# Optimization experiments

Measured on AMD Instinct MI355X. Metric: run time of the kernel, lower is better.

The kernel has to match this reference:

```python
import jax, jax.numpy as jnp
import numpy as np

# Constants matching module reset(): R_reset=5 -> R = 5+15 = 20; T = 10.0; kn=0, gn=1
G = 128          # grid_side
N = G * G        # 16384 cells
R = 20
NB = (2 * R + 3) ** 2        # 1849 = nb_neighbors per the module's assert
NSHIFT = (2 * R + 1) ** 2    # 1681 slots actually filled by the shift loop
T = 10.0
NB_RULES = 4


def _neighbor_idx():
    idx = np.arange(N)
    i, j = idx // G, idx % G
    si, sj = np.meshgrid(np.arange(-R, R + 1), np.arange(-R, R + 1), indexing='ij')
    si, sj = si.ravel(), sj.ravel()   # row-major: shift_i outer loop, shift_j inner
    nb = ((i[:, None] + si[None, :]) % G) * G + (j[:, None] + sj[None, :]) % G  # [N, NSHIFT]
    full = np.zeros((N, NB), dtype=np.int32)   # unfilled slots default to cell 0 (as in torch zeros init)
    full[:, :NSHIFT] = nb
    return jnp.asarray(full)

NEI = _neighbor_idx()   # [N, NB] int32, translation-invariant periodic neighbor list


def setup_inputs() -> dict:
    key = jax.random.key(0)
    ks = jax.random.split(key, 9)
    idx = jnp.arange(N)
    pos = jnp.stack([idx // G, idx % G], axis=-1).astype(jnp.float32)   # [N, 2] grid coords
    x = jax.random.uniform(ks[0], (N, 3), dtype=jnp.float32)            # [N, C] state in [0,1]
    c0 = jax.random.randint(ks[1], (NB_RULES,), 0, 3)                   # source channel per rule
    c1 = jax.random.randint(ks[2], (NB_RULES,), 0, 3)                   # target channel per rule
    r = 0.5 + 0.5 * jax.random.uniform(ks[3], (NB_RULES,), dtype=jnp.float32)
    rk = jax.random.uniform(ks[4], (NB_RULES, 3), dtype=jnp.float32)    # kernel ring centers
    b = jax.random.uniform(ks[5], (NB_RULES, 3), dtype=jnp.float32)     # kernel ring heights
    w = 0.1 + 0.4 * jax.random.uniform(ks[6], (NB_RULES, 3), dtype=jnp.float32)  # ring widths
    h = jax.random.uniform(ks[7], (NB_RULES,), dtype=jnp.float32)       # growth strength
    m = 0.1 + 0.4 * jax.random.uniform(ks[8], (NB_RULES,), dtype=jnp.float32)    # growth mean
    s = 0.05 + 0.1 * jax.random.uniform(jax.random.fold_in(key, 99), (NB_RULES,), dtype=jnp.float32)
    return {"pos": pos, "x": x, "c0": c0, "c1": c1, "r": r, "rk": rk,
            "b": b, "w": w, "h": h, "m": m, "s": s}


def reference(pos, x, c0, c1, r, rk, b, w, h, m, s):
    # gather neighbor states: x_ext[:, 0] is self, rest are the NB neighbors -> [N, 1+NB, C]
    x_ext = jnp.concatenate([x[:, None, :], x[NEI]], axis=1)
    # translation-invariant distance computed at the center cell (as in torch)
    center = G * G // 2 + G // 2
    dpos = jnp.concatenate([jnp.zeros((1, 2), pos.dtype), pos[NEI[center]] - pos[center]], axis=0)  # [1+NB, 2]
    dist = jnp.sqrt(jnp.sum(dpos ** 2, axis=-1)) / R   # [1+NB]
    edge_mask = jax.nn.sigmoid(-(dist - 1.0) * 10.0)
    delta_x = jnp.zeros_like(x)
    for k in range(NB_RULES):
        # kernel_core[0]: sum of Gaussian rings over the last axis
        wk = edge_mask * (b[k] * jnp.exp(-((dist[:, None] / r[k] - rk[k]) / w[k]) ** 2 / 2)).sum(-1)  # [1+NB]
        wn = wk / wk.sum()                    # per-cell weight rows are identical -> compute once
        potential = jnp.mean(wn[None, :] * x_ext[:, :, c0[k]], axis=1)   # aggr='mean' -> [N]
        # field_func[1]
        field = jnp.exp(-(potential - m[k]) ** 2 / (2 * s[k] ** 2) - 0.001) * 2 - 1
        delta_x = delta_x.at[:, c1[k]].add(h[k] * field)
    new_x = jnp.clip(x + delta_x / T, 0.0, 1.0)
    return pos, new_x
```

## Files before the change

### kernel.cpp

```cpp
#include <hip/hip_runtime.h>
#include <math.h>

#define G 128
#define NCELLS (G*G)
#define RAD 20
#define NS 41
#define NTAPS (NS*NS)
#define NB_FULL 1850.0f
#define NTAIL 168.0f
#define NRULES 4
#define NQ 16
#define SROWPAD 44
#define SSZ (NS*SROWPAD)
#define NTILES 16
#define CONV_BLOCKS (NTILES*NRULES*NQ)

#define WOFF_TAIL 0
#define WOFF_STEN 16
#define WOFF_POT  (WOFF_STEN + NRULES*SSZ)

__device__ __forceinline__ float kw(float d, float irk,
                                    float rk0, float rk1, float rk2,
                                    float b0, float b1, float b2,
                                    float iw0, float iw1, float iw2) {
    float em = 1.f / (1.f + __expf((d - 1.f) * 10.f));
    float dd = d * irk;
    float u0 = (dd - rk0) * iw0;
    float u1 = (dd - rk1) * iw1;
    float u2 = (dd - rk2) * iw2;
    return em * (b0 * __expf(-0.5f * u0 * u0)
               + b1 * __expf(-0.5f * u1 * u1)
               + b2 * __expf(-0.5f * u2 * u2));
}

__global__ __launch_bounds__(256)
void lenia_prep(const float* __restrict__ rr,
                const float* __restrict__ rkv,
                const float* __restrict__ bv,
                const float* __restrict__ wv,
                float* __restrict__ ws) {
    __shared__ float red[4];
    const int k = blockIdx.x;
    const int t = threadIdx.x;

    const float irk = 1.f / rr[k];
    const float rk0 = rkv[k*3+0], rk1 = rkv[k*3+1], rk2 = rkv[k*3+2];
    const float b0  = bv[k*3+0],  b1  = bv[k*3+1],  b2  = bv[k*3+2];
    const float iw0 = 1.f / wv[k*3+0], iw1 = 1.f / wv[k*3+1], iw2 = 1.f / wv[k*3+2];
    const float invR = 1.f / (float)RAD;

    float vals[7];
    float lsum = 0.f;
    #pragma unroll
    for (int j = 0; j < 7; ++j) {
        int sidx = t + j * 256;
        float wk = 0.f;
        if (sidx < NTAPS) {
            int si = sidx / NS - RAD;
            int sj = sidx % NS - RAD;
            float d = sqrtf((float)(si*si + sj*sj)) * invR;
            wk = kw(d, irk, rk0, rk1, rk2, b0, b1, b2, iw0, iw1, iw2);
        }
        vals[j] = wk;
        lsum += wk;
    }
    #pragma unroll
    for (int mm = 32; mm > 0; mm >>= 1) lsum += __shfl_xor(lsum, mm, 64);
    if ((t & 63) == 0) red[t >> 6] = lsum;
    __syncthreads();
    const float S4 = red[0] + red[1] + red[2] + red[3];
    const float wself = kw(0.f, irk, rk0, rk1, rk2, b0, b1, b2, iw0, iw1, iw2);
    const float dtail = sqrtf(8192.f) * invR;
    const float wtail = kw(dtail, irk, rk0, rk1, rk2, b0, b1, b2, iw0, iw1, iw2);
    const float S = S4 + wself + NTAIL * wtail;
    const float inv = 1.f / (S * NB_FULL);

    float* st = ws + WOFF_STEN + k * SSZ;
    #pragma unroll
    for (int j = 0; j < 7; ++j) {
        int sidx = t + j * 256;
        if (sidx < NTAPS) {
            float v = vals[j] * inv;
            if (sidx == RAD*NS + RAD) v += wself * inv;
            st[(sidx / NS) * SROWPAD + (sidx % NS)] = v;
        }
    }
    for (int j = t; j < NS * 3; j += 256)
        st[(j / 3) * SROWPAD + NS + (j % 3)] = 0.f;
    if (t == 0) ws[WOFF_TAIL + k] = NTAIL * wtail * inv;
}

#define CROW(rq, wq, wq1)                                                         \
    a0 = fmaf(rq.x, wq.x,  a0); a1 = fmaf(rq.x, wq.y,  a1);                       \
    a2 = fmaf(rq.x, wq.z,  a2); a3 = fmaf(rq.x, wq.w,  a3);                       \
    a0 = fmaf(rq.y, wq.y,  a0); a1 = fmaf(rq.y, wq.z,  a1);                       \
    a2 = fmaf(rq.y, wq.w,  a2); a3 = fmaf(rq.y, wq1.x, a3);                       \
    a0 = fmaf(rq.z, wq.z,  a0); a1 = fmaf(rq.z, wq.w,  a1);                       \
    a2 = fmaf(rq.z, wq1.x, a2); a3 = fmaf(rq.z, wq1.y, a3);                       \
    a0 = fmaf(rq.w, wq.w,  a0); a1 = fmaf(rq.w, wq1.x, a1);                       \
    a2 = fmaf(rq.w, wq1.y, a2); a3 = fmaf(rq.w, wq1.z, a3);

__global__ __launch_bounds__(256, 4)
void lenia_conv(const float* __restrict__ x,
                const int* __restrict__ c0v,
                float* __restrict__ ws) {
    __shared__ __align__(16) float sten[3*SROWPAD];
    __shared__ __align__(16) float xt[10*168];

    const int bid  = blockIdx.x;
    const int q    = bid & 15;
    const int k    = (bid >> 4) & 3;
    const int tile = bid >> 6;
    const int i0   = tile * 8;
    const int t    = threadIdx.x;
    const int nsi  = (q < 9) ? 3 : 2;
    const int si0  = (q < 9) ? 3*q : 27 + 2*(q - 9);
    const int r0   = i0 - RAD + si0;
    const int NR   = nsi + 7;
    const int ck   = c0v[k];

    if (t < nsi * SROWPAD)
        sten[t] = ws[WOFF_STEN + k * SSZ + si0 * SROWPAD + t];

    for (int idx = t; idx < NR * 168; idx += 256) {
        int rrow = idx / 168;
        int cc   = idx - rrow * 168;
        int grow = (r0 + rrow) & (G - 1);
        int gcol = (cc - 20) & (G - 1);
        xt[rrow*168 + cc] = x[grow*(G*3) + gcol*3 + ck];
    }
    __syncthreads();

    const int row = t >> 5;
    const int cb  = (t & 31) * 4;
    float a0 = 0.f, a1 = 0.f, a2 = 0.f, a3 = 0.f;

    #pragma unroll
    for (int ii = 0; ii < 3; ++ii) {
        if (ii < nsi) {
            const float4* wp  = (const float4*)&xt[(row + ii)*168 + cb];
            const float4* rp4 = (const float4*)&sten[ii * SROWPAD];
            float4 w0 = wp[0], w1 = wp[1], w2 = wp[2], w3 = wp[3], w4 = wp[4], w5 = wp[5];
            float4 w6 = wp[6], w7 = wp[7], w8 = wp[8], w9 = wp[9], w10 = wp[10];
            float4 r0v = rp4[0], r1 = rp4[1], r2 = rp4[2], r3 = rp4[3], r4 = rp4[4], r5 = rp4[5];
            float4 r6 = rp4[6], r7 = rp4[7], r8 = rp4[8], r9 = rp4[9], r10 = rp4[10];
            CROW(r0v, w0, w1)  CROW(r1, w1, w2)  CROW(r2, w2, w3)  CROW(r3, w3, w4)
            CROW(r4, w4, w5)  CROW(r5, w5, w6)  CROW(r6, w6, w7)  CROW(r7, w7, w8)
            CROW(r8, w8, w9)  CROW(r9, w9, w10)
            a0 = fmaf(r10.x, w10.x, a0);
            a1 = fmaf(r10.x, w10.y, a1);
            a2 = fmaf(r10.x, w10.z, a2);
            a3 = fmaf(r10.x, w10.w, a3);
        }
    }

    int cell = (i0 + row) * G + cb;
    float4 res; res.x = a0; res.y = a1; res.z = a2; res.w = a3;
    *(float4*)&ws[WOFF_POT + (k * NQ + q) * NCELLS + cell] = res;
}

__global__ __launch_bounds__(128)
void lenia_update(const float* __restrict__ pos,
                  const float* __restrict__ x,
                  const int* __restrict__ c0v,
                  const int* __restrict__ c1v,
                  const float* __restrict__ hv,
                  const float* __restrict__ mv,
                  const float* __restrict__ sv,
                  const float* __restrict__ ws,
                  float* __restrict__ out) {
    int n = blockIdx.x * 128 + threadIdx.x;
    *(float2*)&out[2*n] = *(const float2*)&pos[2*n];

    float xv0 = x[n*3 + 0], xv1 = x[n*3 + 1], xv2 = x[n*3 + 2];
    float d0 = 0.f, d1 = 0.f, d2 = 0.f;
    #pragma unroll
    for (int kk = 0; kk < NRULES; ++kk) {
        float pot = ws[WOFF_TAIL + kk] * x[c0v[kk]];
        #pragma unroll
        for (int qq = 0; qq < NQ; ++qq)
            pot += ws[WOFF_POT + (kk * NQ + qq) * NCELLS + n];
        float u = pot - mv[kk];
        float sk = sv[kk];
        float field = __expf(-u*u / (2.f * sk * sk) - 0.001f) * 2.f - 1.f;
        float add = hv[kk] * field;
        int c = c1v[kk];
        if (c == 0) d0 += add; else if (c == 1) d1 += add; else d2 += add;
    }
    float* ox = out + 2 * NCELLS;
    ox[n*3 + 0] = fminf(fmaxf(xv0 + d0 * 0.1f, 0.f), 1.f);
    ox[n*3 + 1] = fminf(fmaxf(xv1 + d1 * 0.1f, 0.f), 1.f);
    ox[n*3 + 2] = fminf(fmaxf(xv2 + d2 * 0.1f, 0.f), 1.f);
}

extern "C" void kernel_launch(void* const* d_in, const int* in_sizes, int n_in,
                              void* d_out, int out_size, void* d_ws, size_t ws_size,
                              hipStream_t stream) {
    const float* pos = (const float*)d_in[0];
    const float* x   = (const float*)d_in[1];
    const int*   c0  = (const int*)  d_in[2];
    const int*   c1  = (const int*)  d_in[3];
    const float* r   = (const float*)d_in[4];
    const float* rk  = (const float*)d_in[5];
    const float* b   = (const float*)d_in[6];
    const float* w   = (const float*)d_in[7];
    const float* h   = (const float*)d_in[8];
    const float* m   = (const float*)d_in[9];
    const float* s   = (const float*)d_in[10];
    float* out = (float*)d_out;
    float* ws  = (float*)d_ws;

    lenia_prep<<<NRULES, 256, 0, stream>>>(r, rk, b, w, ws);
    lenia_conv<<<CONV_BLOCKS, 256, 0, stream>>>(x, c0, ws);
    lenia_update<<<NCELLS/128, 128, 0, stream>>>(pos, x, c0, c1, h, m, s, ws, out);
}
```

Measured before the change: 26.48 us.

## Deinterleave state into channel planes and load conv tiles with float4

The prep kernel gains extra blocks that transpose the interleaved [N,3] state into three contiguous channel planes in the workspace. The conv kernel then fills its shared tile (including the periodic halo columns) and its stencil rows with float4 loads from the selected plane, replacing scalar strided gathers with integer division. The update kernel's block size is also halved to spread work over more blocks. This adds a workspace write/read pass but aims to cut the load latency and instruction count in the 1024-block conv stage.

```diff
diff --git a/kernel.cpp b/kernel.cpp
--- a/kernel.cpp
+++ b/kernel.cpp
@@ -15,9 +15,10 @@
 #define NTILES 16
 #define CONV_BLOCKS (NTILES*NRULES*NQ)
 
-#define WOFF_TAIL 0
-#define WOFF_STEN 16
-#define WOFF_POT  (WOFF_STEN + NRULES*SSZ)
+#define WOFF_TAIL  0
+#define WOFF_STEN  16
+#define WOFF_POT   (WOFF_STEN + NRULES*SSZ)
+#define WOFF_PLANE (WOFF_POT + NRULES*NQ*NCELLS)
 
 __device__ __forceinline__ float kw(float d, float irk,
                                     float rk0, float rk1, float rk2,
@@ -34,15 +35,28 @@
 }
 
 __global__ __launch_bounds__(256)
-void lenia_prep(const float* __restrict__ rr,
+void lenia_prep(const float* __restrict__ x,
+                const float* __restrict__ rr,
                 const float* __restrict__ rkv,
                 const float* __restrict__ bv,
                 const float* __restrict__ wv,
                 float* __restrict__ ws) {
+    const int bid = blockIdx.x;
+    const int t = threadIdx.x;
+
+    if (bid >= NRULES) {
+        int n = (bid - NRULES) * 256 + t;
+        float v0 = x[n*3 + 0];
+        float v1 = x[n*3 + 1];
+        float v2 = x[n*3 + 2];
+        ws[WOFF_PLANE + 0*NCELLS + n] = v0;
+        ws[WOFF_PLANE + 1*NCELLS + n] = v1;
+        ws[WOFF_PLANE + 2*NCELLS + n] = v2;
+        return;
+    }
+
     __shared__ float red[4];
-    const int k = blockIdx.x;
-    const int t = threadIdx.x;
-
+    const int k = bid;
     const float irk = 1.f / rr[k];
     const float rk0 = rkv[k*3+0], rk1 = rkv[k*3+1], rk2 = rkv[k*3+2];
     const float b0  = bv[k*3+0],  b1  = bv[k*3+1],  b2  = bv[k*3+2];
@@ -101,9 +115,7 @@
     a2 = fmaf(rq.w, wq1.y, a2); a3 = fmaf(rq.w, wq1.z, a3);
 
 __global__ __launch_bounds__(256, 4)
-void lenia_conv(const float* __restrict__ x,
-                const int* __restrict__ c0v,
-                float* __restrict__ ws) {
+void lenia_conv(const int* __restrict__ c0v, float* __restrict__ ws) {
     __shared__ __align__(16) float sten[3*SROWPAD];
     __shared__ __align__(16) float xt[10*168];
 
@@ -119,15 +131,27 @@
     const int NR   = nsi + 7;
     const int ck   = c0v[k];
 
-    if (t < nsi * SROWPAD)
-        sten[t] = ws[WOFF_STEN + k * SSZ + si0 * SROWPAD + t];
-
-    for (int idx = t; idx < NR * 168; idx += 256) {
-        int rrow = idx / 168;
-        int cc   = idx - rrow * 168;
-        int grow = (r0 + rrow) & (G - 1);
-        int gcol = (cc - 20) & (G - 1);
-        xt[rrow*168 + cc] = x[grow*(G*3) + gcol*3 + ck];
+    const float4* xp4 = (const float4*)(ws + WOFF_PLANE + ck * NCELLS);
+    float4* xt4 = (float4*)xt;
+
+    if (t < nsi * 11)
+        ((float4*)sten)[t] = ((const float4*)(ws + WOFF_STEN + k * SSZ))[si0 * 11 + t];
+
+    {
+        int row = t >> 5, lane = t & 31;
+        int grow = (r0 + row) & (G - 1);
+        xt4[row * 42 + 5 + lane] = xp4[grow * 32 + lane];
+        if (t < (NR - 8) * 32) {
+            row = 8 + (t >> 5);
+            grow = (r0 + row) & (G - 1);
+            xt4[row * 42 + 5 + lane] = xp4[grow * 32 + lane];
+        }
+    }
+    if (t < NR * 16) {
+        int row = t >> 4, slot = t & 15;
+        int grow = (r0 + row) & (G - 1);
+        if (slot < 5)        xt4[row * 42 + slot]        = xp4[grow * 32 + 27 + slot];
+        else if (slot < 10)  xt4[row * 42 + 32 + slot]   = xp4[grow * 32 + slot - 5];
     }
     __syncthreads();
 
@@ -159,7 +183,7 @@
     *(float4*)&ws[WOFF_POT + (k * NQ + q) * NCELLS + cell] = res;
 }
 
-__global__ __launch_bounds__(128)
+__global__ __launch_bounds__(64)
 void lenia_update(const float* __restrict__ pos,
                   const float* __restrict__ x,
                   const int* __restrict__ c0v,
@@ -169,7 +193,7 @@
                   const float* __restrict__ sv,
                   const float* __restrict__ ws,
                   float* __restrict__ out) {
-    int n = blockIdx.x * 128 + threadIdx.x;
+    int n = blockIdx.x * 64 + threadIdx.x;
     *(float2*)&out[2*n] = *(const float2*)&pos[2*n];
 
     float xv0 = x[n*3 + 0], xv1 = x[n*3 + 1], xv2 = x[n*3 + 2];
@@ -210,7 +234,7 @@
     float* out = (float*)d_out;
     float* ws  = (float*)d_ws;
 
-    lenia_prep<<<NRULES, 256, 0, stream>>>(r, rk, b, w, ws);
-    lenia_conv<<<CONV_BLOCKS, 256, 0, stream>>>(x, c0, ws);
-    lenia_update<<<NCELLS/128, 128, 0, stream>>>(pos, x, c0, c1, h, m, s, ws, out);
-}
+    lenia_prep<<<NRULES + NCELLS/256, 256, 0, stream>>>(x, r, rk, b, w, ws);
+    lenia_conv<<<CONV_BLOCKS, 256, 0, stream>>>(c0, ws);
+    lenia_update<<<NCELLS/64, 64, 0, stream>>>(pos, x, c0, c1, h, m, s, ws, out);
+}
```

After: 25.57 us. -3.4%, faster.
